# Kernel optimization log

Measured on AMD Instinct MI355X. Metric: run time of the kernel, lower is better.

Reference implementation:

```python
import jax, jax.numpy as jnp
import numpy as np

B, T = 1, 600            # batch_size, seq_len (ms)
U = 10                   # n_bkg_units
N_V1, N_LM = 200000, 50000
NNZ_V1, NNZ_LM = 800000, 200000   # neurons * n_bkg_connections(=4)
LAM = 1000.0 / 1000.0    # bkg_units_firing_rate / 1000 -> Poisson rate per ms


def setup_inputs() -> dict:
    key = jax.random.key(0)
    ks = jax.random.split(key, 7)
    inp = jax.random.normal(ks[0], (B, T, 1), dtype=jnp.float32)
    w_v1 = jax.random.normal(ks[1], (NNZ_V1,), dtype=jnp.float32)
    rows_v1 = jax.random.randint(ks[2], (NNZ_V1,), 0, N_V1, dtype=jnp.int32)
    cols_v1 = jax.random.randint(ks[3], (NNZ_V1,), 0, U, dtype=jnp.int32)
    w_lm = jax.random.normal(ks[4], (NNZ_LM,), dtype=jnp.float32)
    rows_lm = jax.random.randint(ks[5], (NNZ_LM,), 0, N_LM, dtype=jnp.int32)
    cols_lm = jax.random.randint(ks[6], (NNZ_LM,), 0, U, dtype=jnp.int32)
    return {"inp": inp, "w_v1": w_v1, "rows_v1": rows_v1, "cols_v1": cols_v1,
            "w_lm": w_lm, "rows_lm": rows_lm, "cols_lm": cols_lm}


def _column_current(spikes, w, rows, cols, n_neurons):
    # Scatter COO weights into a dense (n_neurons, U) matrix (duplicates sum,
    # matching tf.sparse semantics); U is tiny so this is cheap, then a single
    # GEMM reproduces sparse_dense_matmul(W, spikes^T)^T exactly.
    W = jnp.zeros((n_neurons, U), dtype=spikes.dtype).at[rows, cols].add(w)
    i_in = spikes @ W.T                      # (B*T, n_neurons)
    return i_in.reshape(B, T, n_neurons)


def reference(inp, w_v1, rows_v1, cols_v1, w_lm, rows_lm, cols_lm):
    # Poisson background spikes, fixed key for determinism. inp only sets seq_len.
    pkey = jax.random.key(42)
    spikes = jax.random.poisson(pkey, LAM, (B * T, U)).astype(jnp.float32)
    v1 = _column_current(spikes, w_v1, rows_v1, cols_v1, N_V1)   # (B,T,N_V1)
    lm = _column_current(spikes, w_lm, rows_lm, cols_lm, N_LM)   # (B,T,N_LM)
    return jnp.concatenate([v1, lm], axis=-1)                    # (B,T,N_V1+N_LM)
```

## Files before the change

### kernel.cpp

```cpp
#include <hip/hip_runtime.h>
#include <stdint.h>

#define NV1 200000
#define NLM 50000
#define NTOT 250000
#define TLEN 600
#define UU 10
#define NNZV1 800000
#define NNZLM 200000
#define NNZTOT (NNZV1 + NNZLM)
#define NELEM (TLEN * UU)

#define BINSHIFT 10
#define BINROWS 1024
#define NB 245
#define CAP 4608
#define BBLK 512
#define BPT 8

#define TSPLIT 3
#define TTHIRD (TLEN / TSPLIT)

#define SLOTS_OFF   0ULL
#define SPIKES2_OFF 9031680ULL
#define BINCNT_OFF  9060480ULL
#define WS_NEED_SORT 9061460ULL
#define WT_OFF      0ULL
#define SPIKES_OFF  10000000ULL
#define WS_NEED_FALLBACK 10024000ULL

typedef float f32x4 __attribute__((ext_vector_type(4)));
typedef float f32x2 __attribute__((ext_vector_type(2)));
typedef unsigned long long u64;
typedef u64 u64x2 __attribute__((ext_vector_type(2)));

__device__ __forceinline__ void tf2x32(uint32_t k0, uint32_t k1,
                                       uint32_t c0, uint32_t c1,
                                       uint32_t& o0, uint32_t& o1) {
  const uint32_t ks2 = k0 ^ k1 ^ 0x1BD11BDAu;
  uint32_t x0 = c0 + k0;
  uint32_t x1 = c1 + k1;
#define TF_RND(r) { x0 += x1; x1 = (x1 << (r)) | (x1 >> (32 - (r))); x1 ^= x0; }
  TF_RND(13) TF_RND(15) TF_RND(26) TF_RND(6)
  x0 += k1;  x1 += ks2 + 1u;
  TF_RND(17) TF_RND(29) TF_RND(16) TF_RND(24)
  x0 += ks2; x1 += k0 + 2u;
  TF_RND(13) TF_RND(15) TF_RND(26) TF_RND(6)
  x0 += k0;  x1 += k1 + 3u;
  TF_RND(17) TF_RND(29) TF_RND(16) TF_RND(24)
  x0 += k1;  x1 += ks2 + 4u;
  TF_RND(13) TF_RND(15) TF_RND(26) TF_RND(6)
  x0 += ks2; x1 += k0 + 5u;
#undef TF_RND
  o0 = x0; o1 = x1;
}

__device__ __forceinline__ int spike_value(int e) {
  uint32_t r0 = 0u, r1 = 42u;
  float S = 0.0f;
  int result = 63;
  for (int iter = 0; iter < 64; ++iter) {
    uint32_t n0, n1, s0, s1;
    tf2x32(r0, r1, 0u, 0u, n0, n1);
    tf2x32(r0, r1, 0u, 1u, s0, s1);
    r0 = n0; r1 = n1;
    uint32_t h0, h1;
    tf2x32(s0, s1, 0u, (uint32_t)e, h0, h1);
    const uint32_t bits = h0 ^ h1;
    const float u = __uint_as_float((bits >> 9) | 0x3f800000u) - 1.0f;
    S += logf(u);
    if (!(S > -1.0f)) { result = iter; break; }
  }
  return result;
}

__device__ __forceinline__ void load_nnz(int i,
                                         const float* __restrict__ wv, const int* __restrict__ rv,
                                         const int* __restrict__ cv,
                                         const float* __restrict__ wl, const int* __restrict__ rl,
                                         const int* __restrict__ cl,
                                         int& grow, int& col, float& w) {
  if (i < NNZV1) { grow = rv[i]; col = cv[i]; w = wv[i]; }
  else { const int j = i - NNZV1; grow = NV1 + rl[j]; col = cl[j]; w = wl[j]; }
}

#define SB ((TLEN * 12 + 255) / 256)
__global__ void __launch_bounds__(256) k1_spikes(float* __restrict__ spikes_p,
                                                 uint32_t* __restrict__ binCount) {
  const int gid = blockIdx.x * 256 + threadIdx.x;
  if (gid < NB) binCount[gid] = 0u;
  if (gid < TLEN * 12) {
    const int row = gid / 12, u = gid - row * 12;
    spikes_p[gid] = (u < UU) ? (float)spike_value(row * UU + u) : 0.f;
  }
}

__global__ void __launch_bounds__(256) k3_bin(const float* __restrict__ wv, const int* __restrict__ rv,
                                              const int* __restrict__ cv,
                                              const float* __restrict__ wl, const int* __restrict__ rl,
                                              const int* __restrict__ cl,
                                              uint32_t* __restrict__ binCount,
                                              u64* __restrict__ slots) {
  __shared__ uint32_t hist[256];
  __shared__ uint32_t cur[256];
  const int t = threadIdx.x;
  hist[t] = 0u;
  __syncthreads();
  const int base = blockIdx.x * (256 * BPT);
  u64 pk[BPT];
#pragma unroll
  for (int r = 0; r < BPT; ++r) {
    const int i = base + r * 256 + t;
    pk[r] = ~0ULL;
    if (i < NNZTOT) {
      int grow, col; float w;
      load_nnz(i, wv, rv, cv, wl, rl, cl, grow, col, w);
      pk[r] = ((u64)((uint32_t)grow | ((uint32_t)col << 18)) << 32) |
              (u64)__float_as_uint(w);
      atomicAdd(&hist[grow >> BINSHIFT], 1u);
    }
  }
  __syncthreads();
  if (t < NB) {
    const uint32_t h = hist[t];
    cur[t] = h ? atomicAdd(&binCount[t], h) : 0u;
  }
  __syncthreads();
#pragma unroll
  for (int r = 0; r < BPT; ++r) {
    if (pk[r] != ~0ULL) {
      const uint32_t rc = (uint32_t)(pk[r] >> 32);
      const int bin = (int)((rc & 0x3FFFFu) >> BINSHIFT);
      const uint32_t pos = atomicAdd(&cur[bin], 1u);
      if (pos < CAP) slots[(size_t)bin * CAP + pos] = pk[r];
    }
  }
}

#define SROW 12
__global__ void __launch_bounds__(256) k5_fused(const u64* __restrict__ slots,
                                                const uint32_t* __restrict__ binCount,
                                                const float* __restrict__ spikes_p,
                                                float* __restrict__ out) {
  __shared__ float acc[BINROWS * UU];
  __shared__ float s[TTHIRD * SROW];
  const int t = threadIdx.x;
  const int bin   = blockIdx.x / TSPLIT;
  const int third = blockIdx.x - bin * TSPLIT;
  const int row0 = bin << BINSHIFT;
  const int tt0  = third * TTHIRD;

  for (int i = t; i < BINROWS * UU; i += 256) acc[i] = 0.f;
  {
    const f32x4* src = reinterpret_cast<const f32x4*>(spikes_p + tt0 * SROW);
    f32x4* dst = reinterpret_cast<f32x4*>(s);
    for (int i = t; i < TTHIRD * SROW / 4; i += 256) dst[i] = src[i];
  }
  __syncthreads();

  int cnt = (int)binCount[bin];
  if (cnt > CAP) cnt = CAP;
  const u64* sl = slots + (size_t)bin * CAP;
  for (int i = t * 2; i < cnt; i += 512) {
    if (i + 1 < cnt) {
      const u64x2 vv = *reinterpret_cast<const u64x2*>(&sl[i]);
#pragma unroll
      for (int q = 0; q < 2; ++q) {
        const u64 v = vv[q];
        const uint32_t rc = (uint32_t)(v >> 32);
        atomicAdd(&acc[((int)(rc & 0x3FFFFu) - row0) * UU + (int)(rc >> 18)],
                  __uint_as_float((uint32_t)v));
      }
    } else {
      const u64 v = sl[i];
      const uint32_t rc = (uint32_t)(v >> 32);
      atomicAdd(&acc[((int)(rc & 0x3FFFFu) - row0) * UU + (int)(rc >> 18)],
                __uint_as_float((uint32_t)v));
    }
  }
  __syncthreads();

  const int n = row0 + t * 4;
  if (n >= NTOT) return;
  float w[4][UU];
#pragma unroll
  for (int r = 0; r < 4; ++r)
#pragma unroll
    for (int u = 0; u < UU; ++u)
      w[r][u] = acc[(t * 4 + r) * UU + u];

  float* op = out + (size_t)tt0 * NTOT + n;
  for (int tl = 0; tl < TTHIRD; ++tl) {
    const f32x4 sA = *reinterpret_cast<const f32x4*>(&s[tl * SROW]);
    const f32x4 sB = *reinterpret_cast<const f32x4*>(&s[tl * SROW + 4]);
    const f32x2 sC = *reinterpret_cast<const f32x2*>(&s[tl * SROW + 8]);
    f32x4 a;
#pragma unroll
    for (int r = 0; r < 4; ++r) {
      float x = sA.x * w[r][0];
      x = fmaf(sA.y, w[r][1], x);
      x = fmaf(sA.z, w[r][2], x);
      x = fmaf(sA.w, w[r][3], x);
      x = fmaf(sB.x, w[r][4], x);
      x = fmaf(sB.y, w[r][5], x);
      x = fmaf(sB.z, w[r][6], x);
      x = fmaf(sB.w, w[r][7], x);
      x = fmaf(sC.x, w[r][8], x);
      x = fmaf(sC.y, w[r][9], x);
      a[r] = x;
    }
    __builtin_nontemporal_store(a, reinterpret_cast<f32x4*>(op));
    op += NTOT;
  }
}

#define WZ4 (NTOT * UU / 4)
#define ZB  ((WZ4 + 255) / 256)
#define SBF ((NELEM + 255) / 256)
__global__ void __launch_bounds__(256) init_kernel(f32x4* __restrict__ W4,
                                                   float* __restrict__ spikes) {
  const int b = blockIdx.x;
  if (b < ZB) {
    const int i = b * 256 + threadIdx.x;
    if (i < WZ4) W4[i] = (f32x4)(0.f);
    return;
  }
  const int e = (b - ZB) * 256 + threadIdx.x;
  if (e >= NELEM) return;
  spikes[e] = (float)spike_value(e);
}

__global__ void scatter_kernel(const float* __restrict__ w_v1,
                               const int* __restrict__ rows_v1,
                               const int* __restrict__ cols_v1,
                               const float* __restrict__ w_lm,
                               const int* __restrict__ rows_lm,
                               const int* __restrict__ cols_lm,
                               float* __restrict__ WT) {
  const int i = blockIdx.x * blockDim.x + threadIdx.x;
  if (i >= NNZTOT) return;
  if (i < NNZV1) {
    atomicAdd(&WT[(size_t)cols_v1[i] * NTOT + rows_v1[i]], w_v1[i]);
  } else {
    const int j = i - NNZV1;
    atomicAdd(&WT[(size_t)cols_lm[j] * NTOT + NV1 + rows_lm[j]], w_lm[j]);
  }
}

#define TTILE 75
#define NT4 (NTOT / 4)
__global__ void __launch_bounds__(256, 8) out_kernel(const float* __restrict__ WT,
                                                     const float* __restrict__ spikes,
                                                     float* __restrict__ out) {
  __shared__ float s[TTILE * SROW];
  const int t0 = blockIdx.y * TTILE;
  for (int i = threadIdx.x; i < TTILE * SROW; i += 256) {
    const int row = i / SROW, u = i - row * SROW;
    s[i] = (u < UU) ? spikes[(t0 + row) * UU + u] : 0.f;
  }
  __syncthreads();

  const int n4 = blockIdx.x * 256 + threadIdx.x;
  if (n4 >= NT4) return;
  const int n = n4 * 4;

  f32x4 w[UU];
#pragma unroll
  for (int u = 0; u < UU; ++u)
    w[u] = *reinterpret_cast<const f32x4*>(&WT[(size_t)u * NTOT + n]);

  float* op = &out[(size_t)t0 * NTOT + n];
  for (int t = 0; t < TTILE; ++t) {
    const f32x4 sA = *reinterpret_cast<const f32x4*>(&s[t * SROW]);
    const f32x4 sB = *reinterpret_cast<const f32x4*>(&s[t * SROW + 4]);
    const f32x2 sC = *reinterpret_cast<const f32x2*>(&s[t * SROW + 8]);
    f32x4 acc = sA.x * w[0];
    acc += sA.y * w[1];
    acc += sA.z * w[2];
    acc += sA.w * w[3];
    acc += sB.x * w[4];
    acc += sB.y * w[5];
    acc += sB.z * w[6];
    acc += sB.w * w[7];
    acc += sC.x * w[8];
    acc += sC.y * w[9];
    __builtin_nontemporal_store(acc, reinterpret_cast<f32x4*>(op));
    op += NTOT;
  }
}

extern "C" void kernel_launch(void* const* d_in, const int* in_sizes, int n_in,
                              void* d_out, int out_size, void* d_ws, size_t ws_size,
                              hipStream_t stream) {
  const float* w_v1    = (const float*)d_in[1];
  const int*   rows_v1 = (const int*)d_in[2];
  const int*   cols_v1 = (const int*)d_in[3];
  const float* w_lm    = (const float*)d_in[4];
  const int*   rows_lm = (const int*)d_in[5];
  const int*   cols_lm = (const int*)d_in[6];
  float* out = (float*)d_out;

  char* ws = (char*)d_ws;

  if (ws_size >= WS_NEED_SORT) {
    u64*      slots    = (u64*)(ws + SLOTS_OFF);
    float*    spikes_p = (float*)(ws + SPIKES2_OFF);
    uint32_t* binCount = (uint32_t*)(ws + BINCNT_OFF);
    k1_spikes<<<SB, 256, 0, stream>>>(spikes_p, binCount);
    k3_bin<<<BBLK, 256, 0, stream>>>(w_v1, rows_v1, cols_v1,
                                     w_lm, rows_lm, cols_lm, binCount, slots);
    k5_fused<<<NB * TSPLIT, 256, 0, stream>>>(slots, binCount, spikes_p, out);
  } else if (ws_size >= WS_NEED_FALLBACK) {
    float* WT     = (float*)(ws + WT_OFF);
    float* spikes = (float*)(ws + SPIKES_OFF);
    init_kernel<<<ZB + SBF, 256, 0, stream>>>((f32x4*)WT, spikes);
    scatter_kernel<<<(NNZTOT + 255) / 256, 256, 0, stream>>>(w_v1, rows_v1, cols_v1,
                                                             w_lm, rows_lm, cols_lm, WT);
    dim3 grid((NT4 + 255) / 256, TLEN / TTILE);
    out_kernel<<<grid, 256, 0, stream>>>(WT, spikes, out);
  }
}
```

Measured before the change: 157.6 us.

## Merge time-split blocks into one 512-thread block per bin

Each bin now runs in a single 512-thread block that accumulates the bin's weights once into shared memory. The two 256-thread halves then each write half of the time steps. This removes the triple redundant reading and atomic accumulation of slot data across time-split blocks. The cost is a grid of only 245 blocks, which may underfill the GPU during the store-heavy output phase.

After: 151.3 us, median of 2. 1.04x faster.

```diff
diff --git a/kernel.cpp b/kernel.cpp
--- a/kernel.cpp
+++ b/kernel.cpp
@@ -18,8 +18,7 @@
 #define BBLK 512
 #define BPT 8
 
-#define TSPLIT 3
-#define TTHIRD (TLEN / TSPLIT)
+#define THALF (TLEN / 2)
 
 #define SLOTS_OFF   0ULL
 #define SPIKES2_OFF 9031680ULL
@@ -138,30 +137,28 @@
 }
 
 #define SROW 12
-__global__ void __launch_bounds__(256) k5_fused(const u64* __restrict__ slots,
+__global__ void __launch_bounds__(512) k5_fused(const u64* __restrict__ slots,
                                                 const uint32_t* __restrict__ binCount,
                                                 const float* __restrict__ spikes_p,
                                                 float* __restrict__ out) {
   __shared__ float acc[BINROWS * UU];
-  __shared__ float s[TTHIRD * SROW];
-  const int t = threadIdx.x;
-  const int bin   = blockIdx.x / TSPLIT;
-  const int third = blockIdx.x - bin * TSPLIT;
+  __shared__ float s[TLEN * SROW];
+  const int tid = threadIdx.x;
+  const int bin = blockIdx.x;
   const int row0 = bin << BINSHIFT;
-  const int tt0  = third * TTHIRD;
-
-  for (int i = t; i < BINROWS * UU; i += 256) acc[i] = 0.f;
+
+  for (int i = tid; i < BINROWS * UU; i += 512) acc[i] = 0.f;
   {
-    const f32x4* src = reinterpret_cast<const f32x4*>(spikes_p + tt0 * SROW);
+    const f32x4* src = reinterpret_cast<const f32x4*>(spikes_p);
     f32x4* dst = reinterpret_cast<f32x4*>(s);
-    for (int i = t; i < TTHIRD * SROW / 4; i += 256) dst[i] = src[i];
+    for (int i = tid; i < TLEN * SROW / 4; i += 512) dst[i] = src[i];
   }
   __syncthreads();
 
   int cnt = (int)binCount[bin];
   if (cnt > CAP) cnt = CAP;
   const u64* sl = slots + (size_t)bin * CAP;
-  for (int i = t * 2; i < cnt; i += 512) {
+  for (int i = tid * 2; i < cnt; i += 1024) {
     if (i + 1 < cnt) {
       const u64x2 vv = *reinterpret_cast<const u64x2*>(&sl[i]);
 #pragma unroll
@@ -180,20 +177,24 @@
   }
   __syncthreads();
 
-  const int n = row0 + t * 4;
+  const int t8   = tid & 255;
+  const int half = tid >> 8;
+  const int n = row0 + t8 * 4;
   if (n >= NTOT) return;
   float w[4][UU];
 #pragma unroll
   for (int r = 0; r < 4; ++r)
 #pragma unroll
     for (int u = 0; u < UU; ++u)
-      w[r][u] = acc[(t * 4 + r) * UU + u];
-
+      w[r][u] = acc[(t8 * 4 + r) * UU + u];
+
+  const int tt0 = half * THALF;
   float* op = out + (size_t)tt0 * NTOT + n;
-  for (int tl = 0; tl < TTHIRD; ++tl) {
-    const f32x4 sA = *reinterpret_cast<const f32x4*>(&s[tl * SROW]);
-    const f32x4 sB = *reinterpret_cast<const f32x4*>(&s[tl * SROW + 4]);
-    const f32x2 sC = *reinterpret_cast<const f32x2*>(&s[tl * SROW + 8]);
+  for (int tl = 0; tl < THALF; ++tl) {
+    const int trow = tt0 + tl;
+    const f32x4 sA = *reinterpret_cast<const f32x4*>(&s[trow * SROW]);
+    const f32x4 sB = *reinterpret_cast<const f32x4*>(&s[trow * SROW + 4]);
+    const f32x2 sC = *reinterpret_cast<const f32x2*>(&s[trow * SROW + 8]);
     f32x4 a;
 #pragma unroll
     for (int r = 0; r < 4; ++r) {
@@ -309,7 +310,7 @@
     k1_spikes<<<SB, 256, 0, stream>>>(spikes_p, binCount);
     k3_bin<<<BBLK, 256, 0, stream>>>(w_v1, rows_v1, cols_v1,
                                      w_lm, rows_lm, cols_lm, binCount, slots);
-    k5_fused<<<NB * TSPLIT, 256, 0, stream>>>(slots, binCount, spikes_p, out);
+    k5_fused<<<NB, 512, 0, stream>>>(slots, binCount, spikes_p, out);
   } else if (ws_size >= WS_NEED_FALLBACK) {
     float* WT     = (float*)(ws + WT_OFF);
     float* spikes = (float*)(ws + SPIKES_OFF);
```
